# Performance work log

Measured on AMD Instinct MI355X. Metric: run time of the kernel, lower is better.

## Reference

```python
import jax, jax.numpy as jnp
import numpy as np

DT = 0.4  # simulation time step (env.dt)
EPS = 1e-6


def _second_derivative(x, dt):
    # x: [A, M, T, 2]; central 2nd difference along time axis, zeros at both ends
    # (Derivative2.compute semantics)
    inner = (x[:, :, :-2] - 2.0 * x[:, :, 1:-1] + x[:, :, 2:]) / (dt * dt)
    pad = jnp.zeros_like(x[:, :, :1])
    return jnp.concatenate([pad, inner, pad], axis=2)


def setup_inputs() -> dict:
    key = jax.random.key(0)
    k1, k2, k3 = jax.random.split(key, 3)
    A, M, T = 16, 16, 1024
    ado_states = jax.random.normal(k1, (A, M, T, 2), dtype=jnp.float32)
    ado_states_wo = jax.random.normal(k2, (A, M, T, 2), dtype=jnp.float32)
    partial_grads = jax.random.normal(k3, (T, T, A, 2), dtype=jnp.float32)
    return {"ado_states": ado_states, "ado_states_wo": ado_states_wo,
            "partial_grads": partial_grads}


def reference(ado_states, ado_states_wo, partial_grads):
    T = partial_grads.shape[0]
    ddt = _second_derivative(ado_states, DT)          # [A,M,T,2]
    ddt_wo = _second_derivative(ado_states_wo, DT)    # [A,M,T,2]
    diff = ddt - ddt_wo                               # [A,M,T,2]
    norm = jnp.linalg.norm(diff, axis=3)              # [A,M,T]
    # norm[norm < 1e-6] = inf  ->  1/norm = 0 there
    norm_inv = jnp.where(norm < EPS, 0.0, 1.0 / jnp.where(norm < EPS, 1.0, norm))
    # Broadcast in the original numpy: (A,M)[i,j] * (A,)[j]  (requires A == M).
    # inner(k,t,c) = sum_{i,j} norm_inv[i,j,t] * s[j,t,c] * partials[k,t,j,c]
    w = norm_inv.sum(axis=0)                          # [M==A, T]  (sum over i)
    s = diff.sum(axis=1)                              # [A, T, 2]  (sum over modes)
    ws = w[:, :, None] * s                            # [A, T, 2]
    # partials_x/y(k,t) = pg[k, t-1] - 2*pg[k, t]  (numpy wrap at t-1 = -1)
    partials = jnp.roll(partial_grads, 1, axis=1) - 2.0 * partial_grads  # [T,T,A,2]
    G = jnp.einsum('ktjc,jtc->ktc', partials, ws)     # [T,T,2]
    # accumulate over t in [k-1, T-2] for k in [1, T-1]
    k_idx = jnp.arange(T)[:, None]
    t_idx = jnp.arange(T)[None, :]
    mask = (k_idx >= 1) & (t_idx >= k_idx - 1) & (t_idx <= T - 2)
    per_k = jnp.sum(G * mask[..., None].astype(G.dtype), axis=1)  # [T,2]
    return per_k.reshape(2 * T)  # gradient[2k] = x-part, gradient[2k+1] = y-part
```

## Files before the change

### kernel.cpp

```cpp
#include <hip/hip_runtime.h>
#include <hip/hip_bf16.h>

#define TT 1024
#define AA 16
#define DTS 0.4f
#define EPSV 1e-6f

typedef float f4 __attribute__((ext_vector_type(4)));

__device__ __forceinline__ float2 dd2(const float2* __restrict__ A,
                                      const float2* __restrict__ B,
                                      int row, int t) {
    if (t <= 0 || t >= TT - 1) return make_float2(0.f, 0.f);
    const float2* a = A + row * TT + t;
    const float2* b = B + row * TT + t;
    float2 am = a[-1], a0 = a[0], ap = a[1];
    float2 bm = b[-1], b0 = b[0], bp = b[1];
    const float s = 1.0f / (DTS * DTS);
    float2 r;
    r.x = ((am.x - bm.x) - 2.f * (a0.x - b0.x) + (ap.x - bp.x)) * s;
    r.y = ((am.y - bm.y) - 2.f * (a0.y - b0.y) + (ap.y - bp.y)) * s;
    return r;
}

__global__ __launch_bounds__(256) void wscoef_kernel(const float* __restrict__ ado,
                                                     const float* __restrict__ ado_wo,
                                                     float* __restrict__ ws,
                                                     float* __restrict__ coef,
                                                     float* __restrict__ out) {
    const int bid = blockIdx.x;
    const int tid = threadIdx.x;

    if (bid == 0) {
        #pragma unroll
        for (int i = 0; i < 8; ++i) out[tid + 256 * i] = 0.0f;
    }

    const int j = bid >> 4;
    const int chunk = bid & 15;
    const int sub = tid >> 6;
    const int lane = tid & 63;
    const int t = chunk * 64 + lane;
    const int tb = chunk * 64 + 64;
    const float2* A = (const float2*)ado;
    const float2* B = (const float2*)ado_wo;

    float w = 0.f, sx = 0.f, sy = 0.f;
    float wb = 0.f, sbx = 0.f, sby = 0.f;

    #pragma unroll
    for (int q = 0; q < 4; ++q) {
        int a = sub * 4 + q;
        int rowW = a * AA + j;
        float2 d = dd2(A, B, rowW, t);
        float n = sqrtf(d.x * d.x + d.y * d.y);
        w += (n < EPSV) ? 0.f : 1.f / n;
        int rowS = j * AA + a;
        float2 e = dd2(A, B, rowS, t);
        sx += e.x; sy += e.y;
        if (tb < TT) {
            float2 db = dd2(A, B, rowW, tb);
            float nb = sqrtf(db.x * db.x + db.y * db.y);
            wb += (nb < EPSV) ? 0.f : 1.f / nb;
            float2 eb = dd2(A, B, rowS, tb);
            sbx += eb.x; sby += eb.y;
        }
    }

    __shared__ float lw[4][64], lsx[4][64], lsy[4][64];
    __shared__ float lwb[4], lsbx[4], lsby[4];
    lw[sub][lane] = w; lsx[sub][lane] = sx; lsy[sub][lane] = sy;
    if (lane == 0) { lwb[sub] = wb; lsbx[sub] = sbx; lsby[sub] = sby; }
    __syncthreads();

    if (tid < 64) {
        float W  = lw[0][tid] + lw[1][tid] + lw[2][tid] + lw[3][tid];
        float SX = lsx[0][tid] + lsx[1][tid] + lsx[2][tid] + lsx[3][tid];
        float SY = lsy[0][tid] + lsy[1][tid] + lsy[2][tid] + lsy[3][tid];
        float wsx = W * SX, wsy = W * SY;

        float WB  = lwb[0] + lwb[1] + lwb[2] + lwb[3];
        float wbx = WB * (lsbx[0] + lsbx[1] + lsbx[2] + lsbx[3]);
        float wby = WB * (lsby[0] + lsby[1] + lsby[2] + lsby[3]);

        int tt = chunk * 64 + tid;
        *(float2*)(ws + tt * 32 + j * 2) = make_float2(wsx, wsy);

        float nx = __shfl_down(wsx, 1, 64);
        float ny = __shfl_down(wsy, 1, 64);
        if (tid == 63) { nx = wbx; ny = wby; }
        float cx = nx - 2.f * wsx;
        float cy = ny - 2.f * wsy;
        if (tt == TT - 1) { cx = 0.f; cy = 0.f; }
        *(float2*)(coef + tt * 32 + j * 2) = make_float2(cx, cy);
    }
}

__global__ __launch_bounds__(256, 8) void grad_kernel(const float* __restrict__ pg,
                                                      const float* __restrict__ ws,
                                                      const float* __restrict__ coef,
                                                      float* __restrict__ out) {
    const int g = blockIdx.x;
    const int b = g >> 2;
    const int qi = g & 3;
    const int tid = threadIdx.x;
    __shared__ float red[4][4];

    const int k1 = b + 1;
    const int k2 = TT - 1 - b;
    const bool dup = (k1 == k2);
    const int base1 = (k1 - 1) * 8;
    const int base2 = (k2 - 1) * 8;
    const int n1 = (TT - 1) * 8 - base1;

    const f4* __restrict__ pg4 = (const f4*)pg;
    const f4* __restrict__ coef4 = (const f4*)coef;
    const f4* __restrict__ ws4 = (const f4*)ws;

    float ax1 = 0.f, ay1 = 0.f, ax2 = 0.f, ay2 = 0.f;

    if (qi == 0 && tid < 8) {
        if (k1 >= 2) {
            f4 p  = pg4[(size_t)k1 * 8192 + (k1 - 2) * 8 + tid];
            f4 wv = ws4[(k1 - 1) * 8 + tid];
            ax1 += p.x * wv.x + p.z * wv.z;
            ay1 += p.y * wv.y + p.w * wv.w;
        }
        if (!dup) {
            f4 p  = pg4[(size_t)k2 * 8192 + (k2 - 2) * 8 + tid];
            f4 wv = ws4[(k2 - 1) * 8 + tid];
            ax2 += p.x * wv.x + p.z * wv.z;
            ay2 += p.y * wv.y + p.w * wv.w;
        }
    }

    #pragma unroll
    for (int i = 0; i < 8; ++i) {
        int e = qi * 2048 + tid + 256 * i;
        bool s1 = (e < n1);
        if (s1 || !dup) {
            int q = s1 ? (base1 + e) : (base2 + (e - n1));
            int row = s1 ? k1 : k2;
            f4 p = pg4[(size_t)row * 8192 + q];
            f4 c = coef4[q];
            float px = p.x * c.x + p.z * c.z;
            float py = p.y * c.y + p.w * c.w;
            if (s1) { ax1 += px; ay1 += py; }
            else    { ax2 += px; ay2 += py; }
        }
    }

    for (int off = 32; off > 0; off >>= 1) {
        ax1 += __shfl_down(ax1, off, 64);
        ay1 += __shfl_down(ay1, off, 64);
        ax2 += __shfl_down(ax2, off, 64);
        ay2 += __shfl_down(ay2, off, 64);
    }
    int wave = tid >> 6, lane = tid & 63;
    if (lane == 0) {
        red[wave][0] = ax1; red[wave][1] = ay1;
        red[wave][2] = ax2; red[wave][3] = ay2;
    }
    __syncthreads();
    if (tid < 2 && (tid == 0 || !dup)) {
        float rx = red[0][tid * 2] + red[1][tid * 2] + red[2][tid * 2] + red[3][tid * 2];
        float ry = red[0][tid * 2 + 1] + red[1][tid * 2 + 1] +
                   red[2][tid * 2 + 1] + red[3][tid * 2 + 1];
        int k = tid ? k2 : k1;
        atomicAdd(&out[2 * k + 0], rx);
        atomicAdd(&out[2 * k + 1], ry);
    }
}

extern "C" void kernel_launch(void* const* d_in, const int* in_sizes, int n_in,
                              void* d_out, int out_size, void* d_ws, size_t ws_size,
                              hipStream_t stream) {
    const float* ado    = (const float*)d_in[0];
    const float* ado_wo = (const float*)d_in[1];
    const float* pg     = (const float*)d_in[2];
    float* out  = (float*)d_out;
    float* ws   = (float*)d_ws;
    float* coef = (float*)d_ws + TT * AA * 2;

    wscoef_kernel<<<AA * (TT / 64), 256, 0, stream>>>(ado, ado_wo, ws, coef, out);
    grad_kernel<<<2048, 256, 0, stream>>>(pg, ws, coef, out);
}
```

Baseline: 23.63 us.

## Retile grad kernel into 2D row-block by column-chunk grid and widen wscoef blocks

The gradient kernel now uses a 2D grid. Each block handles 8 consecutive k rows over a 64-column chunk of the triangular region, reuses one coef load across all 8 rows, and exits early for chunks that lie entirely outside the triangle. Diagonal chunks handle the boundary term with a ws-based selection, which replaces the earlier paired-row scheme with its separate boundary load. The wscoef kernel moves to 1024-thread blocks with one row per thread instead of a 4-iteration loop, which increases parallelism but adds a longer shared-memory reduction. Register pressure rises from eight accumulator pairs per thread and eight outstanding loads, and there are more atomic adds per output.

```diff
diff --git a/kernel.cpp b/kernel.cpp
--- a/kernel.cpp
+++ b/kernel.cpp
@@ -23,18 +23,14 @@
     return r;
 }
 
-__global__ __launch_bounds__(256) void wscoef_kernel(const float* __restrict__ ado,
-                                                     const float* __restrict__ ado_wo,
-                                                     float* __restrict__ ws,
-                                                     float* __restrict__ coef,
-                                                     float* __restrict__ out) {
+__global__ __launch_bounds__(1024) void wscoef_kernel(const float* __restrict__ ado,
+                                                      const float* __restrict__ ado_wo,
+                                                      float* __restrict__ ws,
+                                                      float* __restrict__ coef,
+                                                      float* __restrict__ out) {
     const int bid = blockIdx.x;
     const int tid = threadIdx.x;
-
-    if (bid == 0) {
-        #pragma unroll
-        for (int i = 0; i < 8; ++i) out[tid + 256 * i] = 0.0f;
-    }
+    if (bid == 0) { out[tid] = 0.0f; out[tid + 1024] = 0.0f; }
 
     const int j = bid >> 4;
     const int chunk = bid & 15;
@@ -45,43 +41,35 @@
     const float2* A = (const float2*)ado;
     const float2* B = (const float2*)ado_wo;
 
-    float w = 0.f, sx = 0.f, sy = 0.f;
+    float2 d = dd2(A, B, sub * AA + j, t);
+    float n = sqrtf(d.x * d.x + d.y * d.y);
+    float w = (n < EPSV) ? 0.f : 1.f / n;
+    float2 e = dd2(A, B, j * AA + sub, t);
+
     float wb = 0.f, sbx = 0.f, sby = 0.f;
-
-    #pragma unroll
-    for (int q = 0; q < 4; ++q) {
-        int a = sub * 4 + q;
-        int rowW = a * AA + j;
-        float2 d = dd2(A, B, rowW, t);
-        float n = sqrtf(d.x * d.x + d.y * d.y);
-        w += (n < EPSV) ? 0.f : 1.f / n;
-        int rowS = j * AA + a;
-        float2 e = dd2(A, B, rowS, t);
-        sx += e.x; sy += e.y;
-        if (tb < TT) {
-            float2 db = dd2(A, B, rowW, tb);
-            float nb = sqrtf(db.x * db.x + db.y * db.y);
-            wb += (nb < EPSV) ? 0.f : 1.f / nb;
-            float2 eb = dd2(A, B, rowS, tb);
-            sbx += eb.x; sby += eb.y;
-        }
+    if (tb < TT) {
+        float2 db = dd2(A, B, sub * AA + j, tb);
+        float nb = sqrtf(db.x * db.x + db.y * db.y);
+        wb = (nb < EPSV) ? 0.f : 1.f / nb;
+        float2 eb = dd2(A, B, j * AA + sub, tb);
+        sbx = eb.x; sby = eb.y;
     }
 
-    __shared__ float lw[4][64], lsx[4][64], lsy[4][64];
-    __shared__ float lwb[4], lsbx[4], lsby[4];
-    lw[sub][lane] = w; lsx[sub][lane] = sx; lsy[sub][lane] = sy;
+    __shared__ float lw[16][64], lsx[16][64], lsy[16][64];
+    __shared__ float lwb[16], lsbx[16], lsby[16];
+    lw[sub][lane] = w; lsx[sub][lane] = e.x; lsy[sub][lane] = e.y;
     if (lane == 0) { lwb[sub] = wb; lsbx[sub] = sbx; lsby[sub] = sby; }
     __syncthreads();
 
     if (tid < 64) {
-        float W  = lw[0][tid] + lw[1][tid] + lw[2][tid] + lw[3][tid];
-        float SX = lsx[0][tid] + lsx[1][tid] + lsx[2][tid] + lsx[3][tid];
-        float SY = lsy[0][tid] + lsy[1][tid] + lsy[2][tid] + lsy[3][tid];
+        float W = 0.f, SX = 0.f, SY = 0.f, WB = 0.f, BX = 0.f, BY = 0.f;
+        #pragma unroll
+        for (int i = 0; i < 16; ++i) {
+            W += lw[i][tid]; SX += lsx[i][tid]; SY += lsy[i][tid];
+            WB += lwb[i];    BX += lsbx[i];     BY += lsby[i];
+        }
         float wsx = W * SX, wsy = W * SY;
-
-        float WB  = lwb[0] + lwb[1] + lwb[2] + lwb[3];
-        float wbx = WB * (lsbx[0] + lsbx[1] + lsbx[2] + lsbx[3]);
-        float wby = WB * (lsby[0] + lsby[1] + lsby[2] + lsby[3]);
+        float wbx = WB * BX, wby = WB * BY;
 
         int tt = chunk * 64 + tid;
         *(float2*)(ws + tt * 32 + j * 2) = make_float2(wsx, wsy);
@@ -96,79 +84,89 @@
     }
 }
 
-__global__ __launch_bounds__(256, 8) void grad_kernel(const float* __restrict__ pg,
+__global__ __launch_bounds__(256, 2) void grad_kernel(const float* __restrict__ pg,
                                                       const float* __restrict__ ws,
                                                       const float* __restrict__ coef,
                                                       float* __restrict__ out) {
-    const int g = blockIdx.x;
-    const int b = g >> 2;
-    const int qi = g & 3;
+    const int cy = blockIdx.x;
+    const int k0 = blockIdx.y * 8;
+    const int U0 = cy * 64;
+    if (U0 + 65 < k0) return;
+
     const int tid = threadIdx.x;
-    __shared__ float red[4][4];
-
-    const int k1 = b + 1;
-    const int k2 = TT - 1 - b;
-    const bool dup = (k1 == k2);
-    const int base1 = (k1 - 1) * 8;
-    const int base2 = (k2 - 1) * 8;
-    const int n1 = (TT - 1) * 8 - base1;
-
     const f4* __restrict__ pg4 = (const f4*)pg;
     const f4* __restrict__ coef4 = (const f4*)coef;
     const f4* __restrict__ ws4 = (const f4*)ws;
 
-    float ax1 = 0.f, ay1 = 0.f, ax2 = 0.f, ay2 = 0.f;
+    float ax[8], ay[8];
+    #pragma unroll
+    for (int r = 0; r < 8; ++r) { ax[r] = 0.f; ay[r] = 0.f; }
 
-    if (qi == 0 && tid < 8) {
-        if (k1 >= 2) {
-            f4 p  = pg4[(size_t)k1 * 8192 + (k1 - 2) * 8 + tid];
-            f4 wv = ws4[(k1 - 1) * 8 + tid];
-            ax1 += p.x * wv.x + p.z * wv.z;
-            ay1 += p.y * wv.y + p.w * wv.w;
+    const int qbase = cy * 512;
+
+    if (U0 >= k0 + 6) {
+        #pragma unroll
+        for (int i = 0; i < 2; ++i) {
+            const int q = qbase + i * 256 + tid;
+            f4 c = coef4[q];
+            f4 p[8];
+            #pragma unroll
+            for (int r = 0; r < 8; ++r)
+                p[r] = pg4[(size_t)(k0 + r) * 8192 + q];
+            #pragma unroll
+            for (int r = 0; r < 8; ++r) {
+                ax[r] += p[r].x * c.x + p[r].z * c.z;
+                ay[r] += p[r].y * c.y + p[r].w * c.w;
+            }
         }
-        if (!dup) {
-            f4 p  = pg4[(size_t)k2 * 8192 + (k2 - 2) * 8 + tid];
-            f4 wv = ws4[(k2 - 1) * 8 + tid];
-            ax2 += p.x * wv.x + p.z * wv.z;
-            ay2 += p.y * wv.y + p.w * wv.w;
+    } else {
+        #pragma unroll
+        for (int i = 0; i < 2; ++i) {
+            const int q = qbase + i * 256 + tid;
+            const int u = q >> 3;
+            f4 c = coef4[q];
+            f4 wsn;
+            if (q + 8 < 8192) wsn = ws4[q + 8];
+            else { wsn.x = wsn.y = wsn.z = wsn.w = 0.f; }
+            #pragma unroll
+            for (int r = 0; r < 8; ++r) {
+                const int k = k0 + r;
+                if (u + 2 < k) continue;
+                f4 p = pg4[(size_t)k * 8192 + q];
+                float pcx = p.x * c.x + p.z * c.z;
+                float pcy = p.y * c.y + p.w * c.w;
+                float pwx = p.x * wsn.x + p.z * wsn.z;
+                float pwy = p.y * wsn.y + p.w * wsn.w;
+                bool vc = (u >= k - 1);
+                ax[r] += vc ? pcx : pwx;
+                ay[r] += vc ? pcy : pwy;
+            }
         }
     }
 
     #pragma unroll
-    for (int i = 0; i < 8; ++i) {
-        int e = qi * 2048 + tid + 256 * i;
-        bool s1 = (e < n1);
-        if (s1 || !dup) {
-            int q = s1 ? (base1 + e) : (base2 + (e - n1));
-            int row = s1 ? k1 : k2;
-            f4 p = pg4[(size_t)row * 8192 + q];
-            f4 c = coef4[q];
-            float px = p.x * c.x + p.z * c.z;
-            float py = p.y * c.y + p.w * c.w;
-            if (s1) { ax1 += px; ay1 += py; }
-            else    { ax2 += px; ay2 += py; }
+    for (int off = 32; off > 0; off >>= 1) {
+        #pragma unroll
+        for (int r = 0; r < 8; ++r) {
+            ax[r] += __shfl_down(ax[r], off, 64);
+            ay[r] += __shfl_down(ay[r], off, 64);
         }
     }
-
-    for (int off = 32; off > 0; off >>= 1) {
-        ax1 += __shfl_down(ax1, off, 64);
-        ay1 += __shfl_down(ay1, off, 64);
-        ax2 += __shfl_down(ax2, off, 64);
-        ay2 += __shfl_down(ay2, off, 64);
-    }
-    int wave = tid >> 6, lane = tid & 63;
+    __shared__ float red[4][16];
+    const int wave = tid >> 6, lane = tid & 63;
     if (lane == 0) {
-        red[wave][0] = ax1; red[wave][1] = ay1;
-        red[wave][2] = ax2; red[wave][3] = ay2;
+        #pragma unroll
+        for (int r = 0; r < 8; ++r) {
+            red[wave][2 * r + 0] = ax[r];
+            red[wave][2 * r + 1] = ay[r];
+        }
     }
     __syncthreads();
-    if (tid < 2 && (tid == 0 || !dup)) {
-        float rx = red[0][tid * 2] + red[1][tid * 2] + red[2][tid * 2] + red[3][tid * 2];
-        float ry = red[0][tid * 2 + 1] + red[1][tid * 2 + 1] +
-                   red[2][tid * 2 + 1] + red[3][tid * 2 + 1];
-        int k = tid ? k2 : k1;
-        atomicAdd(&out[2 * k + 0], rx);
-        atomicAdd(&out[2 * k + 1], ry);
+    if (tid < 16) {
+        float v = red[0][tid] + red[1][tid] + red[2][tid] + red[3][tid];
+        const int r = tid >> 1, comp = tid & 1;
+        const int k = k0 + r;
+        if (k > 0) atomicAdd(&out[2 * k + comp], v);
     }
 }
 
@@ -182,6 +180,6 @@
     float* ws   = (float*)d_ws;
     float* coef = (float*)d_ws + TT * AA * 2;
 
-    wscoef_kernel<<<AA * (TT / 64), 256, 0, stream>>>(ado, ado_wo, ws, coef, out);
-    grad_kernel<<<2048, 256, 0, stream>>>(pg, ws, coef, out);
+    wscoef_kernel<<<AA * (TT / 64), 1024, 0, stream>>>(ado, ado_wo, ws, coef, out);
+    grad_kernel<<<dim3(16, 128), 256, 0, stream>>>(pg, ws, coef, out);
 }
```

Measured after the change: 26.83 us. 13.5% more time.
